# Kernel optimization log

Hardware: AMD Instinct MI355X
Metric: run time of the kernel (lower is better)

The kernel has to match this reference:

```python
import jax, jax.numpy as jnp
import numpy as np

N, D, H, E, TOPK = 4096, 512, 2048, 8, 2


def setup_inputs() -> dict:
    key = jax.random.key(0)
    k0, k1, k2, k3 = jax.random.split(key, 4)
    scale = 0.02
    return {
        "inp": jax.random.normal(k0, (N, D), jnp.float32),
        "gate_w": jax.random.normal(k1, (D, E), jnp.float32) * scale,
        "gate_b": jnp.zeros((E,), jnp.float32),
        "w1": jax.random.normal(k2, (E, D, H), jnp.float32) * scale,
        "b1": jnp.zeros((E, H), jnp.float32),
        "w2": jax.random.normal(k3, (E, H, D), jnp.float32) * scale,
        "b2": jnp.zeros((E, D), jnp.float32),
        "top_k": TOPK,
    }


def reference(inp, gate_w, gate_b, w1, b1, w2, b2, top_k):
    # --- NaiveGate: linear -> top-k -> softmax over the k selected logits ---
    logits = inp @ gate_w + gate_b                      # [N, E]
    topk_val, topk_idx = jax.lax.top_k(logits, top_k)   # [N, k]
    gate_score = jax.nn.softmax(topk_val, axis=-1)       # [N, k]

    n_tok = inp.shape[0]
    n_exp = gate_w.shape[1]

    # Combine weight per (token, expert): sum of gate scores of slots routed
    # to that expert. Mathematically identical to FastMoE's
    # repeat_interleave -> scatter -> expert_fn -> gather -> bmm(gate_score, x).
    combine = jnp.zeros((n_tok, n_exp), inp.dtype)
    combine = combine.at[jnp.arange(n_tok)[:, None], topk_idx].add(gate_score)

    # --- Experts: 2-layer FFN (d_model -> 4*d_model -> d_model) with GELU ---
    out = jnp.zeros_like(inp)
    for e in range(n_exp):  # small fixed expert count
        h = jax.nn.gelu(inp @ w1[e] + b1[e])             # [N, H]
        y = h @ w2[e] + b2[e]                            # [N, D]
        out = out + combine[:, e:e + 1] * y
    return out
```

## Files before the change

### kernel.cpp

```cpp
#include <hip/hip_runtime.h>
#include <hip/hip_bf16.h>
#include <stdint.h>

#define NTOK 4096
#define DM   512
#define HD   2048
#define NE   8

typedef __bf16 bf16x8 __attribute__((ext_vector_type(8)));
typedef float  f32x4  __attribute__((ext_vector_type(4)));

__device__ __forceinline__ unsigned short f2bf(float f) {
  unsigned int u = __float_as_uint(f);
  u += 0x7FFF + ((u >> 16) & 1);
  return (unsigned short)(u >> 16);
}

__device__ __forceinline__ float gelu_fast(float x) {
  float s = 1.5957691216f * (x + 0.044715f * x * x * x);
  return x / (1.f + __expf(-s));
}

__device__ __forceinline__ void gload_lds16(const void* g, void* l) {
  __builtin_amdgcn_global_load_lds(
      (__attribute__((address_space(1))) const void*)g,
      (__attribute__((address_space(3))) void*)l,
      16, 0, 0);
}

template<int K, int N>
__device__ __forceinline__ void transw_dev(
    const float* __restrict__ in, unsigned short* __restrict__ out,
    int bid, int t, float (*tile)[33]) {
  const int tpe = (K / 32) * (N / 32);
  int e   = bid / tpe;
  int rem = bid % tpe;
  int kt  = rem / (N / 32), nt = rem % (N / 32);
  int tx  = t & 31, ty = t >> 5;
  const float* src = in + ((size_t)e * K + kt * 32) * N + (size_t)nt * 32;
  #pragma unroll
  for (int i = 0; i < 4; i++) {
    int r = ty + i * 8;
    tile[r][tx] = src[(size_t)r * N + tx];
  }
  __syncthreads();
  unsigned short* dst = out + ((size_t)e * N + nt * 32) * K + (size_t)kt * 32;
  #pragma unroll
  for (int i = 0; i < 4; i++) {
    int rr = ty + i * 8;
    dst[(size_t)rr * K + tx] = f2bf(tile[tx][rr]);
  }
}

__global__ __launch_bounds__(256) void prep_kernel(
    const float* __restrict__ inp, const float* __restrict__ w1,
    const float* __restrict__ w2, const float* __restrict__ gw,
    const float* __restrict__ gb, unsigned short* __restrict__ Xb,
    unsigned short* __restrict__ W1T, unsigned short* __restrict__ W2T,
    int* __restrict__ eidx, float* __restrict__ wgtA) {
  __shared__ float tile[32][33];
  const int b = blockIdx.x;
  const int t = threadIdx.x;

  if (b < 1024) {
    int i = b * 256 + t;
    const f32x4* p = (const f32x4*)(inp + (size_t)i * 8);
    f32x4 v0 = p[0], v1 = p[1];
    union { unsigned short s[8]; uint4 u; } o;
    #pragma unroll
    for (int j = 0; j < 4; j++) { o.s[j] = f2bf(v0[j]); o.s[4 + j] = f2bf(v1[j]); }
    *(uint4*)(Xb + (size_t)i * 8) = o.u;
  } else if (b < 9216) {
    transw_dev<DM, HD>(w1, W1T, b - 1024, t, tile);
  } else if (b < 17408) {
    transw_dev<HD, DM>(w2, W2T, b - 9216, t, tile);
  } else {
    int tok = (b - 17408) * 4 + (t >> 6);
    int l   = t & 63;
    const float* x = inp + (size_t)tok * DM;
    float acc[NE];
    #pragma unroll
    for (int e = 0; e < NE; e++) acc[e] = 0.f;
    #pragma unroll
    for (int j = 0; j < DM / 64; j++) {
      int d = j * 64 + l;
      float xv = x[d];
      const float* g = gw + (size_t)d * NE;
      #pragma unroll
      for (int e = 0; e < NE; e++) acc[e] += xv * g[e];
    }
    #pragma unroll
    for (int off = 32; off >= 1; off >>= 1) {
      #pragma unroll
      for (int e = 0; e < NE; e++) acc[e] += __shfl_xor(acc[e], off, 64);
    }
    if (l == 0) {
      float lg[NE];
      #pragma unroll
      for (int e = 0; e < NE; e++) lg[e] = acc[e] + gb[e];
      int i0 = 0;
      #pragma unroll
      for (int e = 1; e < NE; e++) if (lg[e] > lg[i0]) i0 = e;
      int i1 = (i0 == 0) ? 1 : 0;
      #pragma unroll
      for (int e = 0; e < NE; e++) if (e != i0 && lg[e] > lg[i1]) i1 = e;
      float ev = expf(lg[i1] - lg[i0]);
      float w0 = 1.f / (1.f + ev);
      float w1s = ev * w0;
      wgtA[tok * 2]     = w0;
      wgtA[tok * 2 + 1] = w1s;
      eidx[tok * 2]     = i0;
      eidx[tok * 2 + 1] = i1;
    }
  }
}

__global__ __launch_bounds__(256) void build_lists(
    const int* __restrict__ eidx, int* __restrict__ lists,
    int* __restrict__ counts) {
  __shared__ int wsums[4];
  __shared__ int base;
  const int e = blockIdx.x;
  const int t = threadIdx.x;
  const int lane = t & 63, w = t >> 6;
  if (t == 0) base = 0;
  __syncthreads();
  for (int it = 0; it < 2 * NTOK / 256; ++it) {
    int i = it * 256 + t;
    int match = (eidx[i] == e) ? 1 : 0;
    unsigned long long b = __ballot(match);
    int wsum = __popcll(b);
    int lpre = __popcll(b & ((1ull << lane) - 1ull));
    if (lane == 0) wsums[w] = wsum;
    __syncthreads();
    int wpre = 0;
    #pragma unroll
    for (int k = 0; k < 4; k++) if (k < w) wpre += wsums[k];
    int tot = wsums[0] + wsums[1] + wsums[2] + wsums[3];
    if (match) lists[e * NTOK + base + wpre + lpre] = i;
    __syncthreads();
    if (t == 0) base += tot;
    __syncthreads();
  }
  if (t == 0) counts[e] = base;
}

template<int KDIM, int NDIM, bool IS_L1, int KSPLIT>
__global__ __launch_bounds__(512) void moe_gemm(
    const unsigned short* __restrict__ A,
    const unsigned short* __restrict__ WT,
    const float* __restrict__ bias,
    const int* __restrict__ lists,
    const int* __restrict__ counts,
    unsigned short* __restrict__ Hout) {
  __shared__ unsigned short ldsA[256 * 64];
  __shared__ unsigned short ldsB[128 * 64];
  __shared__ int ldsE[256];

  const int CT  = NDIM / 128;
  const int e   = blockIdx.x & 7;
  const int idx = blockIdx.x >> 3;
  const int ct  = idx % CT;
  const int r1  = idx / CT;
  const int ks  = r1 % KSPLIT;
  const int rt  = r1 / KSPLIT;
  const int cnt = counts[e];
  if (rt * 256 >= cnt) return;

  const int t = threadIdx.x;
  if (t < 256) {
    int rg = rt * 256 + t;
    ldsE[t] = lists[e * NTOK + (rg < cnt ? rg : cnt - 1)];
  }
  __syncthreads();

  const int lane = t & 63;
  const int wid  = t >> 6;
  const int wr = wid >> 1, wc = wid & 1;
  const int rowsel = t >> 3;
  const int colsel = (t & 7) ^ (rowsel & 7);

  const int KCH = KDIM / KSPLIT;
  const unsigned short* aptr[4];
  #pragma unroll
  for (int i = 0; i < 4; i++) {
    int rl = i * 64 + rowsel;
    int entry = ldsE[rl];
    long arow = IS_L1 ? (entry >> 1) : entry;
    aptr[i] = A + arow * (long)KDIM + ks * KCH + colsel * 8;
  }
  const unsigned short* bptr[2];
  #pragma unroll
  for (int j = 0; j < 2; j++) {
    int brow = ct * 128 + j * 64 + rowsel;
    bptr[j] = WT + ((long)e * NDIM + brow) * KDIM + ks * KCH + colsel * 8;
  }

  f32x4 acc[4][4] = {};
  const int NKT = KCH / 64;

  for (int kt = 0; kt < NKT; ++kt) {
    #pragma unroll
    for (int i = 0; i < 4; i++)
      gload_lds16(aptr[i] + kt * 64, (char*)ldsA + i * 8192 + t * 16);
    #pragma unroll
    for (int j = 0; j < 2; j++)
      gload_lds16(bptr[j] + kt * 64, (char*)ldsB + j * 8192 + t * 16);
    __syncthreads();
    #pragma unroll
    for (int kk = 0; kk < 2; ++kk) {
      bf16x8 a[4], b[4];
      int ko = kk * 32 + (lane >> 4) * 8;
      #pragma unroll
      for (int m = 0; m < 4; m++) {
        int rx = wr * 64 + m * 16 + (lane & 15);
        a[m] = *(const bf16x8*)&ldsA[rx * 64 + (ko ^ ((rx & 7) << 3))];
      }
      #pragma unroll
      for (int n = 0; n < 4; n++) {
        int rx = wc * 64 + n * 16 + (lane & 15);
        b[n] = *(const bf16x8*)&ldsB[rx * 64 + (ko ^ ((rx & 7) << 3))];
      }
      #pragma unroll
      for (int m = 0; m < 4; m++)
        #pragma unroll
        for (int n = 0; n < 4; n++)
          acc[m][n] = __builtin_amdgcn_mfma_f32_16x16x32_bf16(a[m], b[n], acc[m][n], 0, 0, 0);
    }
    __syncthreads();
  }

  float bv[4];
  #pragma unroll
  for (int n = 0; n < 4; n++)
    bv[n] = IS_L1 ? bias[e * NDIM + ct * 128 + wc * 64 + n * 16 + (lane & 15)] : 0.f;
  unsigned short* ldsO = ldsA;
  unsigned short* Hbase = Hout + (size_t)ks * 8192 * NDIM;

  #pragma unroll
  for (int half = 0; half < 2; ++half) {
    if ((wr >> 1) == half) {
      #pragma unroll
      for (int m = 0; m < 4; m++) {
        int lrow = (wr & 1) * 64 + m * 16 + (lane >> 4) * 4;
        #pragma unroll
        for (int n = 0; n < 4; n++) {
          int col = wc * 64 + n * 16 + (lane & 15);
          #pragma unroll
          for (int r = 0; r < 4; r++) {
            float v = acc[m][n][r] + bv[n];
            ldsO[(lrow + r) * 128 + col] = f2bf(IS_L1 ? gelu_fast(v) : v);
          }
        }
      }
    }
    __syncthreads();
    #pragma unroll
    for (int rnd = 0; rnd < 4; ++rnd) {
      int lrow = rnd * 32 + (t >> 4);
      int row  = half * 128 + lrow;
      if (rt * 256 + row < cnt) {
        int ent = ldsE[row];
        int ch  = t & 15;
        uint4 v = *(const uint4*)&ldsO[lrow * 128 + ch * 8];
        *(uint4*)(Hbase + (size_t)ent * NDIM + ct * 128 + ch * 8) = v;
      }
    }
    __syncthreads();
  }
}

__global__ __launch_bounds__(256) void combine_kernel(
    const unsigned short* __restrict__ Y,
    const float* __restrict__ b2,
    const int* __restrict__ eidx,
    const float* __restrict__ wgtA,
    float* __restrict__ out) {
  const int t   = threadIdx.x;
  const int tok = blockIdx.x * 4 + (t >> 6);
  const int c0  = (t & 63) * 8;
  float o[8] = {};
  #pragma unroll
  for (int slot = 0; slot < 2; ++slot) {
    int ent = tok * 2 + slot;
    int es  = eidx[ent];
    float ws = wgtA[ent];
    uint4 y0 = *(const uint4*)(Y + (size_t)ent * DM + c0);
    uint4 y1 = *(const uint4*)(Y + (size_t)(8192 + ent) * DM + c0);
    const unsigned short* s0 = (const unsigned short*)&y0;
    const unsigned short* s1 = (const unsigned short*)&y1;
    const float* bb = b2 + (size_t)es * DM + c0;
    #pragma unroll
    for (int j = 0; j < 8; j++) {
      float v = __uint_as_float((unsigned)s0[j] << 16)
              + __uint_as_float((unsigned)s1[j] << 16);
      o[j] += ws * (v + bb[j]);
    }
  }
  *(f32x4*)(out + (size_t)tok * DM + c0)     = *(f32x4*)&o[0];
  *(f32x4*)(out + (size_t)tok * DM + c0 + 4) = *(f32x4*)&o[4];
}

extern "C" void kernel_launch(void* const* d_in, const int* in_sizes, int n_in,
                              void* d_out, int out_size, void* d_ws, size_t ws_size,
                              hipStream_t stream) {
  const float* inp = (const float*)d_in[0];
  const float* gw  = (const float*)d_in[1];
  const float* gb  = (const float*)d_in[2];
  const float* w1  = (const float*)d_in[3];
  const float* b1  = (const float*)d_in[4];
  const float* w2  = (const float*)d_in[5];
  const float* b2  = (const float*)d_in[6];
  float* out = (float*)d_out;

  char* ws = (char*)d_ws;
  unsigned short* Xb   = (unsigned short*)(ws + 0);
  unsigned short* W1T  = (unsigned short*)(ws + 4194304);
  unsigned short* W2T  = (unsigned short*)(ws + 20971520);
  unsigned short* Hbuf = (unsigned short*)(ws + 37748736);
  int*   lists  = (int*)  (ws + 71303168);
  float* wgtA   = (float*)(ws + 71434240);
  int*   counts = (int*)  (ws + 71467008);
  int*   eidx   = (int*)  (ws + 71467072);
  unsigned short* Ybuf = (unsigned short*)(ws + 0);

  prep_kernel<<<18432, 256, 0, stream>>>(inp, w1, w2, gw, gb,
                                         Xb, W1T, W2T, eidx, wgtA);
  build_lists<<<NE, 256, 0, stream>>>(eidx, lists, counts);
  moe_gemm<DM, HD, true, 1><<<8 * 32 * (HD / 128), 512, 0, stream>>>(
      Xb, W1T, b1, lists, counts, Hbuf);
  moe_gemm<HD, DM, false, 2><<<8 * 32 * 2 * (DM / 128), 512, 0, stream>>>(
      Hbuf, W2T, b2, lists, counts, Ybuf);
  combine_kernel<<<NTOK / 4, 256, 0, stream>>>(Ybuf, b2, eidx, wgtA, out);
}
```

Measured before the change: 116.3 us.

## Enlarge MoE GEMM tiles to 256x256 with K=128 and 1024-thread blocks

Grows the expert GEMM block tile from 256x128 to 256x256 output and the K step from 64 to 128, using 16 waves per 1024-thread block and about 129 KB of LDS. This doubles operand reuse per LDS load and halves the number of K-loop barriers. The second GEMM's split-K goes from 2 to 4 when the workspace is large enough, with combine summing a variable number of partials. The cost is lower occupancy (one block per CU), fewer blocks for the first GEMM, and extra partial traffic from the wider split-K.

```diff
diff --git a/kernel.cpp b/kernel.cpp
--- a/kernel.cpp
+++ b/kernel.cpp
@@ -146,18 +146,19 @@
 }
 
 template<int KDIM, int NDIM, bool IS_L1, int KSPLIT>
-__global__ __launch_bounds__(512) void moe_gemm(
+__global__ __launch_bounds__(1024) void moe_gemm(
     const unsigned short* __restrict__ A,
     const unsigned short* __restrict__ WT,
     const float* __restrict__ bias,
     const int* __restrict__ lists,
     const int* __restrict__ counts,
     unsigned short* __restrict__ Hout) {
-  __shared__ unsigned short ldsA[256 * 64];
-  __shared__ unsigned short ldsB[128 * 64];
-  __shared__ int ldsE[256];
-
-  const int CT  = NDIM / 128;
+  __shared__ __align__(16) char smem[132096];
+  unsigned short* ldsA = (unsigned short*)smem;
+  unsigned short* ldsB = (unsigned short*)(smem + 65536);
+  int* ldsE = (int*)(smem + 131072);
+
+  const int CT  = NDIM / 256;
   const int e   = blockIdx.x & 7;
   const int idx = blockIdx.x >> 3;
   const int ct  = idx % CT;
@@ -176,50 +177,47 @@
 
   const int lane = t & 63;
   const int wid  = t >> 6;
-  const int wr = wid >> 1, wc = wid & 1;
-  const int rowsel = t >> 3;
-  const int colsel = (t & 7) ^ (rowsel & 7);
+  const int wr = wid >> 2, wc = wid & 3;
+  const int l15 = lane & 15;
+  const int rowsel = t >> 4;
+  const int colsel = (t & 15) ^ (rowsel & 7);
 
   const int KCH = KDIM / KSPLIT;
   const unsigned short* aptr[4];
+  const unsigned short* bptr[4];
   #pragma unroll
   for (int i = 0; i < 4; i++) {
     int rl = i * 64 + rowsel;
     int entry = ldsE[rl];
     long arow = IS_L1 ? (entry >> 1) : entry;
     aptr[i] = A + arow * (long)KDIM + ks * KCH + colsel * 8;
-  }
-  const unsigned short* bptr[2];
-  #pragma unroll
-  for (int j = 0; j < 2; j++) {
-    int brow = ct * 128 + j * 64 + rowsel;
-    bptr[j] = WT + ((long)e * NDIM + brow) * KDIM + ks * KCH + colsel * 8;
+    int brow = ct * 256 + rl;
+    bptr[i] = WT + ((long)e * NDIM + brow) * KDIM + ks * KCH + colsel * 8;
   }
 
   f32x4 acc[4][4] = {};
-  const int NKT = KCH / 64;
+  const int NKT = KCH / 128;
 
   for (int kt = 0; kt < NKT; ++kt) {
     #pragma unroll
-    for (int i = 0; i < 4; i++)
-      gload_lds16(aptr[i] + kt * 64, (char*)ldsA + i * 8192 + t * 16);
-    #pragma unroll
-    for (int j = 0; j < 2; j++)
-      gload_lds16(bptr[j] + kt * 64, (char*)ldsB + j * 8192 + t * 16);
-    __syncthreads();
-    #pragma unroll
-    for (int kk = 0; kk < 2; ++kk) {
+    for (int i = 0; i < 4; i++) {
+      gload_lds16(aptr[i] + kt * 128, smem + i * 16384 + t * 16);
+      gload_lds16(bptr[i] + kt * 128, smem + 65536 + i * 16384 + t * 16);
+    }
+    __syncthreads();
+    #pragma unroll
+    for (int kk = 0; kk < 4; ++kk) {
       bf16x8 a[4], b[4];
       int ko = kk * 32 + (lane >> 4) * 8;
       #pragma unroll
       for (int m = 0; m < 4; m++) {
-        int rx = wr * 64 + m * 16 + (lane & 15);
-        a[m] = *(const bf16x8*)&ldsA[rx * 64 + (ko ^ ((rx & 7) << 3))];
+        int rx = wr * 64 + m * 16 + l15;
+        a[m] = *(const bf16x8*)&ldsA[rx * 128 + (ko ^ ((rx & 7) << 3))];
       }
       #pragma unroll
       for (int n = 0; n < 4; n++) {
-        int rx = wc * 64 + n * 16 + (lane & 15);
-        b[n] = *(const bf16x8*)&ldsB[rx * 64 + (ko ^ ((rx & 7) << 3))];
+        int rx = wc * 64 + n * 16 + l15;
+        b[n] = *(const bf16x8*)&ldsB[rx * 128 + (ko ^ ((rx & 7) << 3))];
       }
       #pragma unroll
       for (int m = 0; m < 4; m++)
@@ -233,43 +231,37 @@
   float bv[4];
   #pragma unroll
   for (int n = 0; n < 4; n++)
-    bv[n] = IS_L1 ? bias[e * NDIM + ct * 128 + wc * 64 + n * 16 + (lane & 15)] : 0.f;
-  unsigned short* ldsO = ldsA;
+    bv[n] = IS_L1 ? bias[e * NDIM + ct * 256 + wc * 64 + n * 16 + l15] : 0.f;
+  unsigned short* ldsO = (unsigned short*)smem;
   unsigned short* Hbase = Hout + (size_t)ks * 8192 * NDIM;
 
   #pragma unroll
-  for (int half = 0; half < 2; ++half) {
-    if ((wr >> 1) == half) {
-      #pragma unroll
-      for (int m = 0; m < 4; m++) {
-        int lrow = (wr & 1) * 64 + m * 16 + (lane >> 4) * 4;
-        #pragma unroll
-        for (int n = 0; n < 4; n++) {
-          int col = wc * 64 + n * 16 + (lane & 15);
-          #pragma unroll
-          for (int r = 0; r < 4; r++) {
-            float v = acc[m][n][r] + bv[n];
-            ldsO[(lrow + r) * 128 + col] = f2bf(IS_L1 ? gelu_fast(v) : v);
-          }
-        }
+  for (int m = 0; m < 4; m++) {
+    int row = wr * 64 + m * 16 + (lane >> 4) * 4;
+    #pragma unroll
+    for (int n = 0; n < 4; n++) {
+      int col = wc * 64 + n * 16 + l15;
+      #pragma unroll
+      for (int r = 0; r < 4; r++) {
+        float v = acc[m][n][r] + bv[n];
+        ldsO[(row + r) * 256 + col] = f2bf(IS_L1 ? gelu_fast(v) : v);
       }
     }
-    __syncthreads();
-    #pragma unroll
-    for (int rnd = 0; rnd < 4; ++rnd) {
-      int lrow = rnd * 32 + (t >> 4);
-      int row  = half * 128 + lrow;
-      if (rt * 256 + row < cnt) {
-        int ent = ldsE[row];
-        int ch  = t & 15;
-        uint4 v = *(const uint4*)&ldsO[lrow * 128 + ch * 8];
-        *(uint4*)(Hbase + (size_t)ent * NDIM + ct * 128 + ch * 8) = v;
-      }
-    }
-    __syncthreads();
-  }
-}
-
+  }
+  __syncthreads();
+
+  #pragma unroll
+  for (int rnd = 0; rnd < 8; ++rnd) {
+    int row = rnd * 32 + (t >> 5);
+    if (rt * 256 + row >= cnt) continue;
+    int ent = ldsE[row];
+    int ch  = t & 31;
+    uint4 v = *(const uint4*)&ldsO[row * 256 + ch * 8];
+    *(uint4*)(Hbase + (size_t)ent * NDIM + ct * 256 + ch * 8) = v;
+  }
+}
+
+template<int NKS>
 __global__ __launch_bounds__(256) void combine_kernel(
     const unsigned short* __restrict__ Y,
     const float* __restrict__ b2,
@@ -285,17 +277,17 @@
     int ent = tok * 2 + slot;
     int es  = eidx[ent];
     float ws = wgtA[ent];
-    uint4 y0 = *(const uint4*)(Y + (size_t)ent * DM + c0);
-    uint4 y1 = *(const uint4*)(Y + (size_t)(8192 + ent) * DM + c0);
-    const unsigned short* s0 = (const unsigned short*)&y0;
-    const unsigned short* s1 = (const unsigned short*)&y1;
+    float v[8] = {};
+    #pragma unroll
+    for (int ks = 0; ks < NKS; ++ks) {
+      uint4 y = *(const uint4*)(Y + ((size_t)ks * 8192 + ent) * DM + c0);
+      const unsigned short* s = (const unsigned short*)&y;
+      #pragma unroll
+      for (int j = 0; j < 8; j++) v[j] += __uint_as_float((unsigned)s[j] << 16);
+    }
     const float* bb = b2 + (size_t)es * DM + c0;
     #pragma unroll
-    for (int j = 0; j < 8; j++) {
-      float v = __uint_as_float((unsigned)s0[j] << 16)
-              + __uint_as_float((unsigned)s1[j] << 16);
-      o[j] += ws * (v + bb[j]);
-    }
+    for (int j = 0; j < 8; j++) o[j] += ws * (v[j] + bb[j]);
   }
   *(f32x4*)(out + (size_t)tok * DM + c0)     = *(f32x4*)&o[0];
   *(f32x4*)(out + (size_t)tok * DM + c0 + 4) = *(f32x4*)&o[4];
@@ -322,14 +314,24 @@
   float* wgtA   = (float*)(ws + 71434240);
   int*   counts = (int*)  (ws + 71467008);
   int*   eidx   = (int*)  (ws + 71467072);
-  unsigned short* Ybuf = (unsigned short*)(ws + 0);
+
+  const size_t yfresh_off = 71499840;
+  const bool bigws = ws_size >= yfresh_off + 4ull * 8192 * 512 * 2;
 
   prep_kernel<<<18432, 256, 0, stream>>>(inp, w1, w2, gw, gb,
                                          Xb, W1T, W2T, eidx, wgtA);
   build_lists<<<NE, 256, 0, stream>>>(eidx, lists, counts);
-  moe_gemm<DM, HD, true, 1><<<8 * 32 * (HD / 128), 512, 0, stream>>>(
+  moe_gemm<DM, HD, true, 1><<<8 * 16 * (HD / 256), 1024, 0, stream>>>(
       Xb, W1T, b1, lists, counts, Hbuf);
-  moe_gemm<HD, DM, false, 2><<<8 * 32 * 2 * (DM / 128), 512, 0, stream>>>(
-      Hbuf, W2T, b2, lists, counts, Ybuf);
-  combine_kernel<<<NTOK / 4, 256, 0, stream>>>(Ybuf, b2, eidx, wgtA, out);
-}
+  if (bigws) {
+    unsigned short* Ybuf = (unsigned short*)(ws + yfresh_off);
+    moe_gemm<HD, DM, false, 4><<<8 * 16 * 4 * (DM / 256), 1024, 0, stream>>>(
+        Hbuf, W2T, b2, lists, counts, Ybuf);
+    combine_kernel<4><<<NTOK / 4, 256, 0, stream>>>(Ybuf, b2, eidx, wgtA, out);
+  } else {
+    unsigned short* Ybuf = (unsigned short*)(ws + 0);
+    moe_gemm<HD, DM, false, 2><<<8 * 16 * 2 * (DM / 256), 1024, 0, stream>>>(
+        Hbuf, W2T, b2, lists, counts, Ybuf);
+    combine_kernel<2><<<NTOK / 4, 256, 0, stream>>>(Ybuf, b2, eidx, wgtA, out);
+  }
+}
```

Result: slower. 156.7 us (+34.7%).
